# Performance work log

Hardware: AMD Instinct MI355X
Metric: run time of the kernel (lower is better)

The kernel has to match this reference:

```python
import jax, jax.numpy as jnp
import numpy as np

BATCH, FEAT = 128, 1024
CLS = 500
HID = 512

def setup_inputs() -> dict:
    key = jax.random.key(0)
    ks = jax.random.split(key, 6)
    return {
        "image_feats": jax.random.normal(ks[0], (BATCH, FEAT), dtype=jnp.float32),
        "attributes": jax.random.normal(ks[1], (CLS, FEAT), dtype=jnp.float32),
        "W1": jax.random.normal(ks[2], (HID, 2 * FEAT), dtype=jnp.float32) * 0.02,
        "b1": jax.random.normal(ks[3], (HID,), dtype=jnp.float32) * 0.02,
        "W2": jax.random.normal(ks[4], (1, HID), dtype=jnp.float32) * 0.02,
        "b2": jax.random.normal(ks[5], (1,), dtype=jnp.float32) * 0.02,
    }

def reference(image_feats, attributes, W1, b1, W2, b2):
    feat_dim = image_feats.shape[1]
    # fc1 on cat([img, attr]) == img @ W1[:, :F].T + attr @ W1[:, F:].T + b1
    # computed via broadcast-add, never materializing the (B, C, 2F) concat.
    img_part = image_feats @ W1[:, :feat_dim].T          # (B, HID)
    attr_part = attributes @ W1[:, feat_dim:].T          # (C, HID)
    h = jax.nn.relu(img_part[:, None, :] + attr_part[None, :, :] + b1)  # (B, C, HID)
    out = jax.nn.sigmoid(jnp.einsum('bch,oh->bco', h, W2) + b2)          # (B, C, 1)
    return out[..., 0]  # (B, C)
```

## Files before the change

### kernel.cpp

```cpp
#include <hip/hip_runtime.h>
#include <math.h>

#define BATCH 128
#define FEAT  1024
#define CLS   500
#define HID   512
#define ISPL  8
#define ASPL  6

constexpr int BM = 64, BN = 64, BK = 16;
constexpr int TB = 16, TC = 16;

constexpr int NIMG  = BATCH * HID;
constexpr int NATTR = CLS * HID;

__global__ __launch_bounds__(256) void gemm_bt_splitk(
    const float* __restrict__ img, const float* __restrict__ attr,
    const float* __restrict__ W1,
    float* __restrict__ imgP, float* __restrict__ attrP)
{
    __shared__ float As[2][BK][BM + 4];
    __shared__ float Bs[2][BK][BN + 4];

    const int t   = threadIdx.x;
    const int bid = blockIdx.x;

    const float* A;
    float* P;
    int M, boff, m0, n0, kt0, nkt;
    if (bid < 128) {
        const int z   = bid >> 4;
        const int rem = bid & 15;
        A = img; P = imgP + (size_t)z * NIMG;
        M = BATCH; boff = 0;
        m0 = (rem >> 3) * BM;
        n0 = (rem & 7) * BN;
        kt0 = z * 8;  nkt = 8;
    } else {
        const int a   = bid - 128;
        const int z   = a / 64;
        const int rem = a & 63;
        A = attr; P = attrP + (size_t)z * NATTR;
        M = CLS; boff = FEAT;
        m0 = (rem >> 3) * BM;
        n0 = (rem & 7) * BN;
        kt0 = (z < 4) ? z * 11 : 44 + (z - 4) * 10;
        nkt = (z < 4) ? 11 : 10;
    }

    const int K   = FEAT;
    const int ldb = 2 * FEAT;

    const int lrow = t >> 2;
    const int lk   = (t & 3) * 4;
    const int tn   = t & 15;
    const int tm   = t >> 4;

    const int mrow = m0 + lrow;
    const bool mok = (mrow < M);
    const float* Aptr = A  + (size_t)mrow * K + lk;
    const float* Bptr = W1 + (size_t)(n0 + lrow) * ldb + boff + lk;

    {
        const int kk = kt0 * BK;
        float4 av = make_float4(0.f, 0.f, 0.f, 0.f);
        if (mok) av = *(const float4*)&Aptr[kk];
        const float4 bv = *(const float4*)&Bptr[kk];
        As[0][lk + 0][lrow] = av.x; As[0][lk + 1][lrow] = av.y;
        As[0][lk + 2][lrow] = av.z; As[0][lk + 3][lrow] = av.w;
        Bs[0][lk + 0][lrow] = bv.x; Bs[0][lk + 1][lrow] = bv.y;
        Bs[0][lk + 2][lrow] = bv.z; Bs[0][lk + 3][lrow] = bv.w;
    }

    float acc[4][4];
    #pragma unroll
    for (int i = 0; i < 4; ++i)
        #pragma unroll
        for (int j = 0; j < 4; ++j) acc[i][j] = 0.f;

    for (int kt = 0; kt < nkt; ++kt) {
        __syncthreads();
        const int cur  = kt & 1;
        const bool more = (kt + 1 < nkt);

        float4 av = make_float4(0.f, 0.f, 0.f, 0.f), bv;
        if (more) {
            const int kk = (kt0 + kt + 1) * BK;
            if (mok) av = *(const float4*)&Aptr[kk];
            bv = *(const float4*)&Bptr[kk];
        }

        #pragma unroll
        for (int k = 0; k < BK; ++k) {
            const float4 a = *(const float4*)&As[cur][k][tm * 4];
            const float4 b = *(const float4*)&Bs[cur][k][tn * 4];
            acc[0][0] = fmaf(a.x, b.x, acc[0][0]);
            acc[0][1] = fmaf(a.x, b.y, acc[0][1]);
            acc[0][2] = fmaf(a.x, b.z, acc[0][2]);
            acc[0][3] = fmaf(a.x, b.w, acc[0][3]);
            acc[1][0] = fmaf(a.y, b.x, acc[1][0]);
            acc[1][1] = fmaf(a.y, b.y, acc[1][1]);
            acc[1][2] = fmaf(a.y, b.z, acc[1][2]);
            acc[1][3] = fmaf(a.y, b.w, acc[1][3]);
            acc[2][0] = fmaf(a.z, b.x, acc[2][0]);
            acc[2][1] = fmaf(a.z, b.y, acc[2][1]);
            acc[2][2] = fmaf(a.z, b.z, acc[2][2]);
            acc[2][3] = fmaf(a.z, b.w, acc[2][3]);
            acc[3][0] = fmaf(a.w, b.x, acc[3][0]);
            acc[3][1] = fmaf(a.w, b.y, acc[3][1]);
            acc[3][2] = fmaf(a.w, b.z, acc[3][2]);
            acc[3][3] = fmaf(a.w, b.w, acc[3][3]);
        }

        if (more) {
            const int nxt = cur ^ 1;
            As[nxt][lk + 0][lrow] = av.x; As[nxt][lk + 1][lrow] = av.y;
            As[nxt][lk + 2][lrow] = av.z; As[nxt][lk + 3][lrow] = av.w;
            Bs[nxt][lk + 0][lrow] = bv.x; Bs[nxt][lk + 1][lrow] = bv.y;
            Bs[nxt][lk + 2][lrow] = bv.z; Bs[nxt][lk + 3][lrow] = bv.w;
        }
    }

    #pragma unroll
    for (int i = 0; i < 4; ++i) {
        const int m = m0 + tm * 4 + i;
        if (m < M) {
            float4 v = make_float4(acc[i][0], acc[i][1], acc[i][2], acc[i][3]);
            *(float4*)&P[(size_t)m * HID + n0 + tn * 4] = v;
        }
    }
}

__global__ __launch_bounds__(256) void merge_kernel(
    const float* __restrict__ imgP, const float* __restrict__ attrP,
    const float* __restrict__ b1,
    float* __restrict__ imgF, float* __restrict__ attrF)
{
    const int g = blockIdx.x * 256 + threadIdx.x;
    const float4* imgP4  = (const float4*)imgP;
    const float4* attrP4 = (const float4*)attrP;
    const float4* b14    = (const float4*)b1;
    if (g < NIMG / 4) {
        float4 s = imgP4[g];
        #pragma unroll
        for (int zz = 1; zz < ISPL; ++zz) {
            const float4 p = imgP4[zz * (NIMG / 4) + g];
            s.x += p.x; s.y += p.y; s.z += p.z; s.w += p.w;
        }
        const float4 bb = b14[g & (HID / 4 - 1)];
        s.x += bb.x; s.y += bb.y; s.z += bb.z; s.w += bb.w;
        ((float4*)imgF)[g] = s;
    } else if (g < NIMG / 4 + NATTR / 4) {
        const int j = g - NIMG / 4;
        float4 s = attrP4[j];
        #pragma unroll
        for (int zz = 1; zz < ASPL; ++zz) {
            const float4 p = attrP4[zz * (NATTR / 4) + j];
            s.x += p.x; s.y += p.y; s.z += p.z; s.w += p.w;
        }
        ((float4*)attrF)[j] = s;
    }
}

__global__ __launch_bounds__(256) void pair_kernel(
    const float* __restrict__ imgF, const float* __restrict__ attrF,
    const float* __restrict__ W2, const float* __restrict__ b2,
    float* __restrict__ out)
{
    __shared__ float U[TB][HID + 4];
    __shared__ float V[TC][HID + 4];
    __shared__ float w2s[HID];

    const int t  = threadIdx.x;
    const int c0 = blockIdx.x * TC;
    const int b0 = blockIdx.y * TB;

    w2s[t]       = W2[t];
    w2s[t + 256] = W2[t + 256];

    #pragma unroll
    for (int rep = 0; rep < 8; ++rep) {
        const int e   = rep * 256 + t;
        const int row = e >> 7;
        const int c4  = (e & 127) * 4;
        *(float4*)&U[row][c4] =
            *(const float4*)&imgF[(b0 + row) * HID + c4];
        const int c = c0 + row;
        float4 v = make_float4(0.f, 0.f, 0.f, 0.f);
        if (c < CLS)
            v = *(const float4*)&attrF[c * HID + c4];
        *(float4*)&V[row][c4] = v;
    }
    __syncthreads();

    const int ci = t & 15;
    const int bi = t >> 4;

    float acc = 0.f;
    #pragma unroll 16
    for (int h4 = 0; h4 < HID / 4; ++h4) {
        const float4 u = *(const float4*)&U[bi][h4 * 4];
        const float4 v = *(const float4*)&V[ci][h4 * 4];
        const float4 w = *(const float4*)&w2s[h4 * 4];
        acc = fmaf(fmaxf(u.x + v.x, 0.f), w.x, acc);
        acc = fmaf(fmaxf(u.y + v.y, 0.f), w.y, acc);
        acc = fmaf(fmaxf(u.z + v.z, 0.f), w.z, acc);
        acc = fmaf(fmaxf(u.w + v.w, 0.f), w.w, acc);
    }

    const int b = b0 + bi;
    const int c = c0 + ci;
    if (c < CLS) {
        const float x = acc + b2[0];
        out[b * CLS + c] = 1.f / (1.f + __expf(-x));
    }
}

extern "C" void kernel_launch(void* const* d_in, const int* in_sizes, int n_in,
                              void* d_out, int out_size, void* d_ws, size_t ws_size,
                              hipStream_t stream) {
    const float* img  = (const float*)d_in[0];
    const float* attr = (const float*)d_in[1];
    const float* W1   = (const float*)d_in[2];
    const float* b1   = (const float*)d_in[3];
    const float* W2   = (const float*)d_in[4];
    const float* b2   = (const float*)d_in[5];
    float* out = (float*)d_out;

    float* ws    = (float*)d_ws;
    float* imgP  = ws;
    float* attrP = imgP  + (size_t)ISPL * NIMG;
    float* imgF  = attrP + (size_t)ASPL * NATTR;
    float* attrF = imgF  + (size_t)NIMG;

    gemm_bt_splitk<<<dim3(512), 256, 0, stream>>>(img, attr, W1, imgP, attrP);

    const int n4 = NIMG / 4 + NATTR / 4;
    merge_kernel<<<(n4 + 255) / 256, 256, 0, stream>>>(imgP, attrP, b1, imgF, attrF);

    dim3 pgrid((CLS + TC - 1) / TC, BATCH / TB);
    pair_kernel<<<pgrid, 256, 0, stream>>>(imgF, attrF, W2, b2, out);
}
```

Before: 93.95 us.

## Register-block pair kernel over classes and split hidden dim across wave groups

Each thread in the pair kernel now computes 4 classes for one batch row over a quarter of the hidden dimension, reusing each loaded U and w2 float4 across four V rows. The four hidden-dimension partials are combined through a small shared-memory reduction before the sigmoid. The aim is to cut LDS loads per FMA in the dominant pairwise loop. The cost is an extra barrier, a little more shared memory, and only a quarter of the threads doing the epilogue.

```diff
diff --git a/kernel.cpp b/kernel.cpp
--- a/kernel.cpp
+++ b/kernel.cpp
@@ -170,6 +170,7 @@
     __shared__ float U[TB][HID + 4];
     __shared__ float V[TC][HID + 4];
     __shared__ float w2s[HID];
+    __shared__ float red[4][TB][TC];
 
     const int t  = threadIdx.x;
     const int c0 = blockIdx.x * TC;
@@ -193,26 +194,62 @@
     }
     __syncthreads();
 
-    const int ci = t & 15;
-    const int bi = t >> 4;
-
-    float acc = 0.f;
-    #pragma unroll 16
-    for (int h4 = 0; h4 < HID / 4; ++h4) {
-        const float4 u = *(const float4*)&U[bi][h4 * 4];
-        const float4 v = *(const float4*)&V[ci][h4 * 4];
-        const float4 w = *(const float4*)&w2s[h4 * 4];
-        acc = fmaf(fmaxf(u.x + v.x, 0.f), w.x, acc);
-        acc = fmaf(fmaxf(u.y + v.y, 0.f), w.y, acc);
-        acc = fmaf(fmaxf(u.z + v.z, 0.f), w.z, acc);
-        acc = fmaf(fmaxf(u.w + v.w, 0.f), w.w, acc);
-    }
-
-    const int b = b0 + bi;
-    const int c = c0 + ci;
-    if (c < CLS) {
-        const float x = acc + b2[0];
-        out[b * CLS + c] = 1.f / (1.f + __expf(-x));
+    const int q  = t >> 6;
+    const int bi = (t >> 2) & 15;
+    const int cg = t & 3;
+
+    float4 acc4 = make_float4(0.f, 0.f, 0.f, 0.f);
+
+    #pragma unroll 8
+    for (int i = 0; i < HID / 4 / 4; ++i) {
+        const int h = (q * 32 + i) * 4;
+        const float4 u  = *(const float4*)&U[bi][h];
+        const float4 w  = *(const float4*)&w2s[h];
+        const float4 v0 = *(const float4*)&V[cg * 4 + 0][h];
+        const float4 v1 = *(const float4*)&V[cg * 4 + 1][h];
+        const float4 v2 = *(const float4*)&V[cg * 4 + 2][h];
+        const float4 v3 = *(const float4*)&V[cg * 4 + 3][h];
+
+        acc4.x = fmaf(fmaxf(u.x + v0.x, 0.f), w.x, acc4.x);
+        acc4.x = fmaf(fmaxf(u.y + v0.y, 0.f), w.y, acc4.x);
+        acc4.x = fmaf(fmaxf(u.z + v0.z, 0.f), w.z, acc4.x);
+        acc4.x = fmaf(fmaxf(u.w + v0.w, 0.f), w.w, acc4.x);
+
+        acc4.y = fmaf(fmaxf(u.x + v1.x, 0.f), w.x, acc4.y);
+        acc4.y = fmaf(fmaxf(u.y + v1.y, 0.f), w.y, acc4.y);
+        acc4.y = fmaf(fmaxf(u.z + v1.z, 0.f), w.z, acc4.y);
+        acc4.y = fmaf(fmaxf(u.w + v1.w, 0.f), w.w, acc4.y);
+
+        acc4.z = fmaf(fmaxf(u.x + v2.x, 0.f), w.x, acc4.z);
+        acc4.z = fmaf(fmaxf(u.y + v2.y, 0.f), w.y, acc4.z);
+        acc4.z = fmaf(fmaxf(u.z + v2.z, 0.f), w.z, acc4.z);
+        acc4.z = fmaf(fmaxf(u.w + v2.w, 0.f), w.w, acc4.z);
+
+        acc4.w = fmaf(fmaxf(u.x + v3.x, 0.f), w.x, acc4.w);
+        acc4.w = fmaf(fmaxf(u.y + v3.y, 0.f), w.y, acc4.w);
+        acc4.w = fmaf(fmaxf(u.z + v3.z, 0.f), w.z, acc4.w);
+        acc4.w = fmaf(fmaxf(u.w + v3.w, 0.f), w.w, acc4.w);
+    }
+
+    if (q != 0) *(float4*)&red[q][bi][cg * 4] = acc4;
+    __syncthreads();
+
+    if (q == 0) {
+        #pragma unroll
+        for (int qq = 1; qq < 4; ++qq) {
+            const float4 r = *(const float4*)&red[qq][bi][cg * 4];
+            acc4.x += r.x; acc4.y += r.y; acc4.z += r.z; acc4.w += r.w;
+        }
+        const int b  = b0 + bi;
+        const int c  = c0 + cg * 4;
+        const float bb = b2[0];
+        const float vals[4] = {acc4.x, acc4.y, acc4.z, acc4.w};
+        #pragma unroll
+        for (int j = 0; j < 4; ++j) {
+            if (c + j < CLS)
+                out[b * CLS + c + j] =
+                    1.f / (1.f + __expf(-(vals[j] + bb)));
+        }
     }
 }
 
```

Measured after the change: 92.18 us. About the same (-1.9%).
